# Performance work log

Hardware: AMD Instinct MI355X
Metric: run time of the kernel (lower is better)

The kernel has to match this reference:

```python
import jax, jax.numpy as jnp
import numpy as np

L_, H_, D_, GRP_ = 16, 16, 64, 4  # num_layers, num_heads, dims, conv groups factor


def setup_inputs() -> dict:
    key = jax.random.key(0)
    k1, k2, k3 = jax.random.split(key, 3)
    B, K, n, E = 4, 4, 256, 768
    G = GRP_ * L_ * 2                      # 128 conv groups
    Cin_g = E * L_ * 2 // G                # 192 in-channels per group
    Cout_g = H_ * D_ * L_ * 2 // G         # 256 out-channels per group
    rng = np.random.default_rng(0)
    lengths = rng.integers(n // 2, n + 1, size=B * K)
    mask = (np.arange(n)[None, :] < lengths[:, None]).astype(np.int32)
    last_hidden = jax.random.normal(k1, (B * K, n, E), jnp.float32) * 0.02
    weight = jax.random.normal(k2, (G, Cout_g, Cin_g), jnp.float32) * 0.02
    bias = jax.random.normal(k3, (G * Cout_g,), jnp.float32) * 0.02
    return {"last_hidden": last_hidden, "attention_mask": jnp.asarray(mask),
            "weight": weight, "bias": bias, "k": K}


def _forward(last_hidden, weight, bias, mask_np, k):
    Bk, n, E = last_hidden.shape
    B = Bk // k
    G = weight.shape[0]
    # mean pooling over valid tokens
    mask_f = jnp.asarray(mask_np).astype(last_hidden.dtype)
    pooled = (last_hidden * mask_f[..., None]).sum(1) / mask_f.sum(1)[..., None]
    # tile along feature dim (L*2 copies), move channels first: [Bk, E*2L, n]
    x = jnp.tile(last_hidden, (1, 1, 2 * L_)).transpose(0, 2, 1)
    x = x.reshape(Bk, G, -1, n)  # [Bk, G, Cin/G, n]
    # grouped 1x1 conv == per-group GEMM
    y = jnp.einsum('bgin,goi->bgon', x, weight).reshape(Bk, -1, n) + bias[None, :, None]
    # [B, k, L, 2, D, H, n] -> permute(0,1,2,3,5,6,4) -> [B, k, L, 2, H, n, D]
    y = y.reshape(B, k, L_, 2, D_, H_, n).transpose(0, 1, 2, 3, 5, 6, 4)
    # bring (k, n) together for ragged gather: [B, k*n, L, 2, H, D]
    y = y.transpose(0, 1, 5, 2, 3, 4, 6).reshape(B, k * n, L_, 2, H_, D_)
    lens = mask_np.sum(1).reshape(B, k)
    Tmax = int(lens.sum(1).max())
    idx = np.zeros((B, Tmax), np.int32)
    valid = np.zeros((B, Tmax), np.int32)
    for i in range(B):  # tiny host-side loop over B to build gather map
        pos = np.concatenate([j * n + np.arange(lens[i, j]) for j in range(k)])
        idx[i, :pos.size] = pos
        valid[i, :pos.size] = 1
    batch = y[jnp.arange(B)[:, None], jnp.asarray(idx)]  # [B, Tmax, L, 2, H, D]
    batch = batch * jnp.asarray(valid)[:, :, None, None, None, None].astype(batch.dtype)
    batch = batch.transpose(2, 3, 0, 4, 1, 5)  # [L, 2, B, H, Tmax, D]
    return pooled, batch, jnp.asarray(valid, jnp.int32)


def reference(last_hidden, attention_mask, weight, bias, k):
    mask_np = np.asarray(attention_mask)
    return _forward(last_hidden, weight, bias, mask_np, k)
```

## Files before the change

### kernel.cpp

```cpp
#include <hip/hip_runtime.h>
#include <hip/hip_bf16.h>


typedef float f32x4 __attribute__((ext_vector_type(4)));
typedef __bf16 bf16x8 __attribute__((ext_vector_type(8)));
typedef unsigned short u16x4 __attribute__((ext_vector_type(4)));
typedef unsigned short u16x8 __attribute__((ext_vector_type(8)));

__device__ __forceinline__ unsigned short f2bf(float f) {
    union { float f; unsigned u; } v; v.f = f;
    unsigned r = v.u + 0x7FFFu + ((v.u >> 16) & 1u);
    return (unsigned short)(r >> 16);
}

__device__ __forceinline__ bf16x8 ldfrag(const unsigned short* p) {
    u16x8 r = *(const u16x8*)p;
    return __builtin_bit_cast(bf16x8, r);
}

__global__ void cums_kernel(const int* __restrict__ mask, int* __restrict__ ws,
                            float* __restrict__ valid_out, int Tmax) {
    int tid = threadIdx.x;
    int w = tid >> 6, lane = tid & 63;
    int m = mask[w * 256 + lane] + mask[w * 256 + lane + 64] +
            mask[w * 256 + lane + 128] + mask[w * 256 + lane + 192];
#pragma unroll
    for (int off = 32; off > 0; off >>= 1) m += __shfl_down(m, off);
    if (lane == 0) ws[w] = m;
    __syncthreads();
    if (tid == 0) {
        for (int b = 0; b < 4; ++b) {
            int c = 0;
            for (int j = 0; j < 4; ++j) { ws[16 + b * 4 + j] = c; c += ws[b * 4 + j]; }
            ws[32 + b] = c;
        }
    }
    __syncthreads();
    for (int i = tid; i < 4 * Tmax; i += 1024) {
        int b = i / Tmax;
        int T = i - b * Tmax;
        valid_out[i] = (T < ws[32 + b]) ? 1.0f : 0.0f;
    }
}

__global__ void pooled_kernel(const float* __restrict__ lh, const int* __restrict__ mask,
                              const int* __restrict__ ws, float* __restrict__ pooled) {
    int bs = blockIdx.x / 12;
    int ec = blockIdx.x - bs * 12;
    int tid = threadIdx.x;
    int tg = tid >> 6, lane = tid & 63;
    int e = ec * 64 + lane;
    float s = 0.f;
    for (int t = tg; t < 256; t += 4) {
        float mf = (float)mask[bs * 256 + t];
        s += lh[(size_t)(bs * 256 + t) * 768 + e] * mf;
    }
    __shared__ float red[4][64];
    red[tg][lane] = s;
    __syncthreads();
    if (tg == 0) {
        float tot = red[0][lane] + red[1][lane] + red[2][lane] + red[3][lane];
        pooled[bs * 768 + e] = tot / (float)ws[bs];
    }
}

__global__ void packall_kernel(const float* __restrict__ wgt, const float* __restrict__ lh,
                               unsigned short* __restrict__ Wp, unsigned short* __restrict__ Lp) {
    int bid = blockIdx.x;
    if (bid < 3072) {
        int ls = bid / 96;
        int rem = bid - ls * 96;
        int kk = rem >> 4;
        int blk = rem & 15;
        int slot = (blk << 8) + threadIdx.x;
        int row = slot >> 2;
        int sc = slot & 3;
        int coloff = (sc ^ ((row >> 1) & 3)) << 3;
        const float* src = wgt + (size_t)ls * 196608 + row * 192 + (kk << 5) + coloff;
        f32x4 a0 = *(const f32x4*)src;
        f32x4 a1 = *(const f32x4*)(src + 4);
        u16x8 w = { f2bf(a0[0]), f2bf(a0[1]), f2bf(a0[2]), f2bf(a0[3]),
                    f2bf(a1[0]), f2bf(a1[1]), f2bf(a1[2]), f2bf(a1[3]) };
        *(u16x8*)(Wp + (((size_t)(ls * 6 + kk) << 12) + slot) * 8) = w;
    } else {
        size_t slot = (size_t)(bid - 3072) * 256 + threadIdx.x;
        const float* src = lh + slot * 8;
        f32x4 a0 = *(const f32x4*)src;
        f32x4 a1 = *(const f32x4*)(src + 4);
        u16x8 w = { f2bf(a0[0]), f2bf(a0[1]), f2bf(a0[2]), f2bf(a0[3]),
                    f2bf(a1[0]), f2bf(a1[1]), f2bf(a1[2]), f2bf(a1[3]) };
        *(u16x8*)(Lp + slot * 8) = w;
    }
}

__global__ __launch_bounds__(512, 4) void gemm_t(
    const unsigned short* __restrict__ Wp, const unsigned short* __restrict__ Lp,
    const float* __restrict__ bias, const int* __restrict__ ws,
    float* __restrict__ out, int Tmax, int nT) {
    __shared__ __align__(16) unsigned short As[1024][32];
    __shared__ __align__(16) float biasT[16][64];

    int x = blockIdx.x;
    int xcd = x & 7;
    int rest = x >> 3;
    int per = nT << 2;
    int lsq = rest / per;
    int j = rest - lsq * per;
    int ls = (lsq << 3) + xcd;
    int b = j / nT;
    int Tt = j - b * nT;
    int Tbase = Tt << 5;

    int total = ws[32 + b];
    int tid = threadIdx.x;
    int lane = tid & 63;
    int wv = tid >> 6;
    int toff = lane & 3, dcq = lane >> 2;
    float* batch = out + 12288;
    size_t hd0 = (size_t)((ls << 2) + b) << 4;

    if (Tbase >= total) {
        f32x4 z = {0.f, 0.f, 0.f, 0.f};
#pragma unroll
        for (int r = 0; r < 4; ++r) {
#pragma unroll
            for (int gi = 0; gi < 4; ++gi) {
                int flat = (wv << 2) + gi;
                int hq = flat >> 3, t4 = flat & 7;
                int tglob = Tbase + (t4 << 2) + toff;
                int h = (hq << 2) + r;
                if (tglob < Tmax) {
                    float* dst = batch + ((hd0 + h) * (size_t)Tmax + tglob) * 64;
                    *(f32x4*)(dst + (dcq << 2)) = z;
                }
            }
        }
        return;
    }

    {
        int i0 = tid, i1 = tid + 512;
        biasT[i0 & 15][((i0 >> 8) << 4) + ((i0 & 255) >> 4)] = bias[(ls << 10) + i0];
        biasT[i1 & 15][((i1 >> 8) << 4) + ((i1 & 255) >> 4)] = bias[(ls << 10) + i1];
    }

    int beta = wv >> 1, oh = wv & 1;
    int p = lane & 15, q = lane >> 4;

    int c1 = ws[16 + (b << 2) + 1];
    int c2 = ws[16 + (b << 2) + 2];
    int c3 = ws[16 + (b << 2) + 3];
    const unsigned short* Brow[2];
    bool bval[2];
#pragma unroll
    for (int n = 0; n < 2; ++n) {
        int Ti = Tbase + (n << 4) + p;
        bval[n] = Ti < total;
        int TiC = bval[n] ? Ti : (total - 1);
        int sj = (TiC >= c1) + (TiC >= c2) + (TiC >= c3);
        int cum = sj == 0 ? 0 : (sj == 1 ? c1 : (sj == 2 ? c2 : c3));
        int row = ((b << 2) + sj) * 256 + (TiC - cum);
        Brow[n] = Lp + (size_t)row * 768 + beta * 192 + (q << 3);
    }

    f32x4 acc[8][2] = {};
    const bf16x8 bz = {};

    const char* gpanel = (const char*)Wp + (((size_t)(ls * 6)) << 16) + (wv << 13) + (lane << 4);
    char* lbase = ((char*)&As[0][0]) + (wv << 13);

#pragma unroll
    for (int cc = 0; cc < 6; ++cc) {
        asm volatile("s_waitcnt lgkmcnt(0)" ::: "memory");
        __builtin_amdgcn_sched_barrier(0);
        const char* g = gpanel + ((size_t)cc << 16);
#pragma unroll
        for (int it = 0; it < 8; ++it)
            __builtin_amdgcn_global_load_lds(
                (const __attribute__((address_space(1))) void*)(g + it * 1024),
                (__attribute__((address_space(3))) void*)(lbase + it * 1024), 16, 0, 0);
        bf16x8 bf0 = bval[0] ? ldfrag(Brow[0] + (cc << 5)) : bz;
        bf16x8 bf1 = bval[1] ? ldfrag(Brow[1] + (cc << 5)) : bz;
        asm volatile("s_waitcnt vmcnt(0)" ::: "memory");
        __builtin_amdgcn_sched_barrier(0);
#pragma unroll
        for (int r8 = 0; r8 < 8; ++r8) {
            int row = (wv << 7) + (r8 << 4) + p;
            bf16x8 af = ldfrag(&As[row][(q ^ ((row >> 1) & 3)) << 3]);
            acc[r8][0] = __builtin_amdgcn_mfma_f32_16x16x32_bf16(af, bf0, acc[r8][0], 0, 0, 0);
            acc[r8][1] = __builtin_amdgcn_mfma_f32_16x16x32_bf16(af, bf1, acc[r8][1], 0, 0, 0);
        }
    }

    __syncthreads();

    float* Ltr = (float*)&As[0][0];
    int col0 = (beta << 4) + (oh << 3);

#pragma unroll
    for (int r = 0; r < 4; ++r) {
#pragma unroll
        for (int n = 0; n < 2; ++n) {
            int rowL = (((n << 4) + p) << 2) + q;
            f32x4 v0 = { acc[0][n][r], acc[1][n][r], acc[2][n][r], acc[3][n][r] };
            f32x4 v1 = { acc[4][n][r], acc[5][n][r], acc[6][n][r], acc[7][n][r] };
            *(f32x4*)(Ltr + rowL * 68 + col0) = v0;
            *(f32x4*)(Ltr + rowL * 68 + col0 + 4) = v1;
        }
        __syncthreads();
#pragma unroll
        for (int gi = 0; gi < 4; ++gi) {
            int flat = (wv << 2) + gi;
            int hq = flat >> 3, t4 = flat & 7;
            int tloc = (t4 << 2) + toff;
            int h = (hq << 2) + r;
            int tglob = Tbase + tloc;
            if (tglob < Tmax) {
                f32x4 v;
                if (tglob < total) {
                    v = *(const f32x4*)(Ltr + ((tloc << 2) + hq) * 68 + (dcq << 2));
                    v += *(const f32x4*)&biasT[h][dcq << 2];
                } else {
                    v = (f32x4){0.f, 0.f, 0.f, 0.f};
                }
                float* dst = batch + ((hd0 + h) * (size_t)Tmax + tglob) * 64;
                *(f32x4*)(dst + (dcq << 2)) = v;
            }
        }
        __syncthreads();
    }
}

__global__ void zerotail_kernel(float* __restrict__ batch, const int* __restrict__ ws,
                                int Tmax) {
    int rr = blockIdx.x;
    int b = rr >> 9;
    int rem = rr & 511;
    int l = rem >> 5, s = (rem >> 4) & 1, h = rem & 15;
    int total = ws[32 + b];
    int span = Tmax - total;
    if (span <= 0) return;
    float* row = batch + (((size_t)((l * 2 + s) * 4 + b) * 16 + h) * (size_t)Tmax + total) * 64;
    f32x4 z = {0.f, 0.f, 0.f, 0.f};
    int nchunk = span << 4;
    for (int j = threadIdx.x; j < nchunk; j += 256)
        *(f32x4*)(row + (j << 2)) = z;
}

__global__ __launch_bounds__(512, 4) void gemm_fb(
    const float* __restrict__ lh, const float* __restrict__ wgt,
    const float* __restrict__ bias, const int* __restrict__ ws,
    float* __restrict__ out, int Tmax) {
    __shared__ __align__(16) unsigned short As[1024][32];
    __shared__ __align__(16) float biasT[16][64];

    int x = blockIdx.x;
    int xcd = x & 7;
    int rest = x >> 3;
    int lsq = rest >> 7;
    int rb = rest & 127;
    int ls = (lsq << 3) + xcd;
    int bs = rb >> 3;
    int tq = rb & 7;

    int len = ws[bs];
    int tbase = tq << 5;
    if (tbase >= len) return;

    int tid = threadIdx.x;
    {
        int i0 = tid, i1 = tid + 512;
        biasT[i0 & 15][((i0 >> 8) << 4) + ((i0 & 255) >> 4)] = bias[(ls << 10) + i0];
        biasT[i1 & 15][((i1 >> 8) << 4) + ((i1 & 255) >> 4)] = bias[(ls << 10) + i1];
    }

    int lane = tid & 63;
    int wv = tid >> 6;
    int beta = wv >> 1, oh = wv & 1;
    int p = lane & 15, q = lane >> 4;

    f32x4 acc[8][2] = {};

#pragma unroll
    for (int cc = 0; cc < 6; ++cc) {
        const int kk = cc << 5;
        const float* Awg = wgt + (size_t)ls * 196608;
        int arow0 = tid >> 2;
        int achk = tid & 3;
#pragma unroll
        for (int it = 0; it < 8; ++it) {
            int row = arow0 + (it << 7);
            const float* src = Awg + row * 192 + kk + (achk << 3);
            f32x4 a0 = *(const f32x4*)src;
            f32x4 a1 = *(const f32x4*)(src + 4);
            u16x8 aw = { f2bf(a0[0]), f2bf(a0[1]), f2bf(a0[2]), f2bf(a0[3]),
                         f2bf(a1[0]), f2bf(a1[1]), f2bf(a1[2]), f2bf(a1[3]) };
            *(u16x8*)&As[row][(achk ^ ((row >> 1) & 3)) << 3] = aw;
        }
        bf16x8 bf[2];
        const float* Brow = lh + (size_t)bs * 196608 + (size_t)(tbase + p) * 768 +
                            beta * 192 + (q << 3) + kk;
#pragma unroll
        for (int n = 0; n < 2; ++n) {
            const float* bp = Brow + n * 16 * 768;
            f32x4 b0 = *(const f32x4*)bp;
            f32x4 b1 = *(const f32x4*)(bp + 4);
            u16x8 bw = { f2bf(b0[0]), f2bf(b0[1]), f2bf(b0[2]), f2bf(b0[3]),
                         f2bf(b1[0]), f2bf(b1[1]), f2bf(b1[2]), f2bf(b1[3]) };
            bf[n] = __builtin_bit_cast(bf16x8, bw);
        }
        __syncthreads();
#pragma unroll
        for (int r8 = 0; r8 < 8; ++r8) {
            int row = (beta << 8) + (oh << 7) + (r8 << 4) + p;
            bf16x8 af = ldfrag(&As[row][(q ^ ((row >> 1) & 3)) << 3]);
            acc[r8][0] = __builtin_amdgcn_mfma_f32_16x16x32_bf16(af, bf[0], acc[r8][0], 0, 0, 0);
            acc[r8][1] = __builtin_amdgcn_mfma_f32_16x16x32_bf16(af, bf[1], acc[r8][1], 0, 0, 0);
        }
        __syncthreads();
    }

    float* Ltr = (float*)&As[0][0];
    int cum = ws[16 + bs];
    int b = bs >> 2;
    float* batch = out + 12288;
    size_t hd0 = (size_t)((ls << 2) + b) << 4;

    int toff = lane & 3, dcq = lane >> 2;
    int col0 = (beta << 4) + (oh << 3);

#pragma unroll
    for (int r = 0; r < 4; ++r) {
#pragma unroll
        for (int n = 0; n < 2; ++n) {
            int rowL = (((n << 4) + p) << 2) + q;
            f32x4 v0 = { acc[0][n][r], acc[1][n][r], acc[2][n][r], acc[3][n][r] };
            f32x4 v1 = { acc[4][n][r], acc[5][n][r], acc[6][n][r], acc[7][n][r] };
            *(f32x4*)(Ltr + rowL * 68 + col0) = v0;
            *(f32x4*)(Ltr + rowL * 68 + col0 + 4) = v1;
        }
        __syncthreads();
#pragma unroll
        for (int gi = 0; gi < 4; ++gi) {
            int flat = (wv << 2) + gi;
            int hq = flat >> 3, t4 = flat & 7;
            int tloc = (t4 << 2) + toff;
            int h = (hq << 2) + r;
            int tglob = tbase + tloc;
            f32x4 v = *(const f32x4*)(Ltr + ((tloc << 2) + hq) * 68 + (dcq << 2));
            v += *(const f32x4*)&biasT[h][dcq << 2];
            if (tglob < len) {
                float* dst = batch + ((hd0 + h) * (size_t)Tmax + cum + tglob) * 64;
                *(f32x4*)(dst + (dcq << 2)) = v;
            }
        }
        __syncthreads();
    }
}

extern "C" void kernel_launch(void* const* d_in, const int* in_sizes, int n_in,
                              void* d_out, int out_size, void* d_ws, size_t ws_size,
                              hipStream_t stream) {
    const float* lh   = (const float*)d_in[0];
    const int*   mask = (const int*)d_in[1];
    const float* wgt  = (const float*)d_in[2];
    const float* bias = (const float*)d_in[3];
    float* out = (float*)d_out;
    int* ws = (int*)d_ws;

    int Tmax = (out_size - 12288) / 131076;
    int nT = (Tmax + 31) >> 5;

    unsigned short* Wp = (unsigned short*)((char*)d_ws + 1024);
    unsigned short* Lp = (unsigned short*)((char*)d_ws + 1024 + 12582912);
    const size_t need = 1024 + 12582912 + 6291456;
    bool packed = ws_size >= need;

    cums_kernel<<<1, 1024, 0, stream>>>(mask, ws, out + 12288 + (size_t)131072 * Tmax, Tmax);
    pooled_kernel<<<16 * 12, 256, 0, stream>>>(lh, mask, ws, out);

    if (packed) {
        packall_kernel<<<4608, 256, 0, stream>>>(wgt, lh, Wp, Lp);
        gemm_t<<<128 * nT, 512, 0, stream>>>(Wp, Lp, bias, ws, out, Tmax, nT);
    } else {
        zerotail_kernel<<<2048, 256, 0, stream>>>(out + 12288, ws, Tmax);
        gemm_fb<<<4096, 512, 0, stream>>>(lh, wgt, bias, ws, out, Tmax);
    }
}
```

Baseline: 192.4 us.

## Merge prep kernels into one launch and software-pipeline GEMM K-loop loads

The mask cumsum, pooled mean and bf16 pack kernels are merged into a single prep launch, so three launches become one. The pooled branch now derives each sequence length from the mask itself instead of reading ws written by another block. The GEMM K loop is restructured to prefetch the next B fragment and issue the next A panel's global-to-LDS load after the current MFMAs, overlapping memory with compute. Risk: the LDS buffer is reused without a barrier between waves, so correctness depends on each wave only touching its own slice.

```diff
diff --git a/kernel.cpp b/kernel.cpp
--- a/kernel.cpp
+++ b/kernel.cpp
@@ -18,61 +18,29 @@
     return __builtin_bit_cast(bf16x8, r);
 }
 
-__global__ void cums_kernel(const int* __restrict__ mask, int* __restrict__ ws,
+__device__ __forceinline__ bf16x8 ldfrag_masked(const unsigned short* p, bool valid) {
+    u16x8 r = *(const u16x8*)p;
+    u16x8 z = {};
+    r = valid ? r : z;
+    return __builtin_bit_cast(bf16x8, r);
+}
+
+__global__ void prep_kernel(const float* __restrict__ wgt, const float* __restrict__ lh,
+                            const int* __restrict__ mask,
+                            unsigned short* __restrict__ Wp, unsigned short* __restrict__ Lp,
+                            int* __restrict__ ws, float* __restrict__ pooled,
                             float* __restrict__ valid_out, int Tmax) {
+    __shared__ float red[4][64];
+    __shared__ float mred[4];
+    int bid = blockIdx.x;
     int tid = threadIdx.x;
-    int w = tid >> 6, lane = tid & 63;
-    int m = mask[w * 256 + lane] + mask[w * 256 + lane + 64] +
-            mask[w * 256 + lane + 128] + mask[w * 256 + lane + 192];
-#pragma unroll
-    for (int off = 32; off > 0; off >>= 1) m += __shfl_down(m, off);
-    if (lane == 0) ws[w] = m;
-    __syncthreads();
-    if (tid == 0) {
-        for (int b = 0; b < 4; ++b) {
-            int c = 0;
-            for (int j = 0; j < 4; ++j) { ws[16 + b * 4 + j] = c; c += ws[b * 4 + j]; }
-            ws[32 + b] = c;
-        }
-    }
-    __syncthreads();
-    for (int i = tid; i < 4 * Tmax; i += 1024) {
-        int b = i / Tmax;
-        int T = i - b * Tmax;
-        valid_out[i] = (T < ws[32 + b]) ? 1.0f : 0.0f;
-    }
-}
-
-__global__ void pooled_kernel(const float* __restrict__ lh, const int* __restrict__ mask,
-                              const int* __restrict__ ws, float* __restrict__ pooled) {
-    int bs = blockIdx.x / 12;
-    int ec = blockIdx.x - bs * 12;
-    int tid = threadIdx.x;
-    int tg = tid >> 6, lane = tid & 63;
-    int e = ec * 64 + lane;
-    float s = 0.f;
-    for (int t = tg; t < 256; t += 4) {
-        float mf = (float)mask[bs * 256 + t];
-        s += lh[(size_t)(bs * 256 + t) * 768 + e] * mf;
-    }
-    __shared__ float red[4][64];
-    red[tg][lane] = s;
-    __syncthreads();
-    if (tg == 0) {
-        float tot = red[0][lane] + red[1][lane] + red[2][lane] + red[3][lane];
-        pooled[bs * 768 + e] = tot / (float)ws[bs];
-    }
-}
-
-__global__ void packall_kernel(const float* __restrict__ wgt, const float* __restrict__ lh,
-                               unsigned short* __restrict__ Wp, unsigned short* __restrict__ Lp) {
-    int bid = blockIdx.x;
+
     if (bid < 3072) {
         int ls = bid / 96;
         int rem = bid - ls * 96;
         int kk = rem >> 4;
         int blk = rem & 15;
-        int slot = (blk << 8) + threadIdx.x;
+        int slot = (blk << 8) + tid;
         int row = slot >> 2;
         int sc = slot & 3;
         int coloff = (sc ^ ((row >> 1) & 3)) << 3;
@@ -82,14 +50,56 @@
         u16x8 w = { f2bf(a0[0]), f2bf(a0[1]), f2bf(a0[2]), f2bf(a0[3]),
                     f2bf(a1[0]), f2bf(a1[1]), f2bf(a1[2]), f2bf(a1[3]) };
         *(u16x8*)(Wp + (((size_t)(ls * 6 + kk) << 12) + slot) * 8) = w;
-    } else {
-        size_t slot = (size_t)(bid - 3072) * 256 + threadIdx.x;
+    } else if (bid < 4608) {
+        size_t slot = (size_t)(bid - 3072) * 256 + tid;
         const float* src = lh + slot * 8;
         f32x4 a0 = *(const f32x4*)src;
         f32x4 a1 = *(const f32x4*)(src + 4);
         u16x8 w = { f2bf(a0[0]), f2bf(a0[1]), f2bf(a0[2]), f2bf(a0[3]),
                     f2bf(a1[0]), f2bf(a1[1]), f2bf(a1[2]), f2bf(a1[3]) };
         *(u16x8*)(Lp + slot * 8) = w;
+    } else if (bid < 4800) {
+        int r = bid - 4608;
+        int bs = r / 12, ec = r - bs * 12;
+        int tg = tid >> 6, lane = tid & 63;
+        int e = ec * 64 + lane;
+        float s = 0.f, mc = 0.f;
+        for (int t = tg; t < 256; t += 4) {
+            float mf = (float)mask[bs * 256 + t];
+            s += lh[(size_t)(bs * 256 + t) * 768 + e] * mf;
+            mc += mf;
+        }
+        red[tg][lane] = s;
+        if (lane == 0) mred[tg] = mc;
+        __syncthreads();
+        if (tg == 0) {
+            float tot = red[0][lane] + red[1][lane] + red[2][lane] + red[3][lane];
+            float len = mred[0] + mred[1] + mred[2] + mred[3];
+            pooled[bs * 768 + e] = tot / len;
+        }
+    } else {
+        int w = tid >> 6, lane = tid & 63;
+        for (int bs = w; bs < 16; bs += 4) {
+            int m = mask[bs * 256 + lane] + mask[bs * 256 + lane + 64] +
+                    mask[bs * 256 + lane + 128] + mask[bs * 256 + lane + 192];
+#pragma unroll
+            for (int off = 32; off > 0; off >>= 1) m += __shfl_down(m, off);
+            if (lane == 0) ws[bs] = m;
+        }
+        __syncthreads();
+        if (tid == 0) {
+            for (int b = 0; b < 4; ++b) {
+                int c = 0;
+                for (int j = 0; j < 4; ++j) { ws[16 + b * 4 + j] = c; c += ws[b * 4 + j]; }
+                ws[32 + b] = c;
+            }
+        }
+        __syncthreads();
+        for (int i = tid; i < 4 * Tmax; i += 256) {
+            int b = i / Tmax;
+            int T = i - b * Tmax;
+            valid_out[i] = (T < ws[32 + b]) ? 1.0f : 0.0f;
+        }
     }
 }
 
@@ -138,6 +148,14 @@
         return;
     }
 
+    const char* gpanel = (const char*)Wp + (((size_t)(ls * 6)) << 16) + (wv << 13) + (lane << 4);
+    char* lbase = ((char*)&As[0][0]) + (wv << 13);
+#pragma unroll
+    for (int it = 0; it < 8; ++it)
+        __builtin_amdgcn_global_load_lds(
+            (const __attribute__((address_space(1))) void*)(gpanel + it * 1024),
+            (__attribute__((address_space(3))) void*)(lbase + it * 1024), 16, 0, 0);
+
     {
         int i0 = tid, i1 = tid + 512;
         biasT[i0 & 15][((i0 >> 8) << 4) + ((i0 & 255) >> 4)] = bias[(ls << 10) + i0];
@@ -166,30 +184,38 @@
     f32x4 acc[8][2] = {};
     const bf16x8 bz = {};
 
-    const char* gpanel = (const char*)Wp + (((size_t)(ls * 6)) << 16) + (wv << 13) + (lane << 4);
-    char* lbase = ((char*)&As[0][0]) + (wv << 13);
+    bf16x8 bc0 = ldfrag_masked(Brow[0], bval[0]);
+    bf16x8 bc1 = ldfrag_masked(Brow[1], bval[1]);
 
 #pragma unroll
     for (int cc = 0; cc < 6; ++cc) {
-        asm volatile("s_waitcnt lgkmcnt(0)" ::: "memory");
-        __builtin_amdgcn_sched_barrier(0);
-        const char* g = gpanel + ((size_t)cc << 16);
-#pragma unroll
-        for (int it = 0; it < 8; ++it)
-            __builtin_amdgcn_global_load_lds(
-                (const __attribute__((address_space(1))) void*)(g + it * 1024),
-                (__attribute__((address_space(3))) void*)(lbase + it * 1024), 16, 0, 0);
-        bf16x8 bf0 = bval[0] ? ldfrag(Brow[0] + (cc << 5)) : bz;
-        bf16x8 bf1 = bval[1] ? ldfrag(Brow[1] + (cc << 5)) : bz;
-        asm volatile("s_waitcnt vmcnt(0)" ::: "memory");
+        bf16x8 bn0 = bz, bn1 = bz;
+        if (cc < 5) {
+            bn0 = ldfrag_masked(Brow[0] + ((cc + 1) << 5), bval[0]);
+            bn1 = ldfrag_masked(Brow[1] + ((cc + 1) << 5), bval[1]);
+            asm volatile("s_waitcnt vmcnt(2)" ::: "memory");
+        } else {
+            asm volatile("s_waitcnt vmcnt(0)" ::: "memory");
+        }
         __builtin_amdgcn_sched_barrier(0);
 #pragma unroll
         for (int r8 = 0; r8 < 8; ++r8) {
             int row = (wv << 7) + (r8 << 4) + p;
             bf16x8 af = ldfrag(&As[row][(q ^ ((row >> 1) & 3)) << 3]);
-            acc[r8][0] = __builtin_amdgcn_mfma_f32_16x16x32_bf16(af, bf0, acc[r8][0], 0, 0, 0);
-            acc[r8][1] = __builtin_amdgcn_mfma_f32_16x16x32_bf16(af, bf1, acc[r8][1], 0, 0, 0);
-        }
+            acc[r8][0] = __builtin_amdgcn_mfma_f32_16x16x32_bf16(af, bc0, acc[r8][0], 0, 0, 0);
+            acc[r8][1] = __builtin_amdgcn_mfma_f32_16x16x32_bf16(af, bc1, acc[r8][1], 0, 0, 0);
+        }
+        if (cc < 5) {
+            asm volatile("s_waitcnt lgkmcnt(0)" ::: "memory");
+            __builtin_amdgcn_sched_barrier(0);
+            const char* g = gpanel + ((size_t)(cc + 1) << 16);
+#pragma unroll
+            for (int it = 0; it < 8; ++it)
+                __builtin_amdgcn_global_load_lds(
+                    (const __attribute__((address_space(1))) void*)(g + it * 1024),
+                    (__attribute__((address_space(3))) void*)(lbase + it * 1024), 16, 0, 0);
+        }
+        bc0 = bn0; bc1 = bn1;
     }
 
     __syncthreads();
@@ -231,6 +257,52 @@
     }
 }
 
+__global__ void cums_kernel(const int* __restrict__ mask, int* __restrict__ ws,
+                            float* __restrict__ valid_out, int Tmax) {
+    int tid = threadIdx.x;
+    int w = tid >> 6, lane = tid & 63;
+    int m = mask[w * 256 + lane] + mask[w * 256 + lane + 64] +
+            mask[w * 256 + lane + 128] + mask[w * 256 + lane + 192];
+#pragma unroll
+    for (int off = 32; off > 0; off >>= 1) m += __shfl_down(m, off);
+    if (lane == 0) ws[w] = m;
+    __syncthreads();
+    if (tid == 0) {
+        for (int b = 0; b < 4; ++b) {
+            int c = 0;
+            for (int j = 0; j < 4; ++j) { ws[16 + b * 4 + j] = c; c += ws[b * 4 + j]; }
+            ws[32 + b] = c;
+        }
+    }
+    __syncthreads();
+    for (int i = tid; i < 4 * Tmax; i += 1024) {
+        int b = i / Tmax;
+        int T = i - b * Tmax;
+        valid_out[i] = (T < ws[32 + b]) ? 1.0f : 0.0f;
+    }
+}
+
+__global__ void pooled_kernel(const float* __restrict__ lh, const int* __restrict__ mask,
+                              const int* __restrict__ ws, float* __restrict__ pooled) {
+    int bs = blockIdx.x / 12;
+    int ec = blockIdx.x - bs * 12;
+    int tid = threadIdx.x;
+    int tg = tid >> 6, lane = tid & 63;
+    int e = ec * 64 + lane;
+    float s = 0.f;
+    for (int t = tg; t < 256; t += 4) {
+        float mf = (float)mask[bs * 256 + t];
+        s += lh[(size_t)(bs * 256 + t) * 768 + e] * mf;
+    }
+    __shared__ float red[4][64];
+    red[tg][lane] = s;
+    __syncthreads();
+    if (tg == 0) {
+        float tot = red[0][lane] + red[1][lane] + red[2][lane] + red[3][lane];
+        pooled[bs * 768 + e] = tot / (float)ws[bs];
+    }
+}
+
 __global__ void zerotail_kernel(float* __restrict__ batch, const int* __restrict__ ws,
                                 int Tmax) {
     int rr = blockIdx.x;
@@ -376,13 +448,14 @@
     const size_t need = 1024 + 12582912 + 6291456;
     bool packed = ws_size >= need;
 
-    cums_kernel<<<1, 1024, 0, stream>>>(mask, ws, out + 12288 + (size_t)131072 * Tmax, Tmax);
-    pooled_kernel<<<16 * 12, 256, 0, stream>>>(lh, mask, ws, out);
+    float* valid_out = out + 12288 + (size_t)131072 * Tmax;
 
     if (packed) {
-        packall_kernel<<<4608, 256, 0, stream>>>(wgt, lh, Wp, Lp);
+        prep_kernel<<<4801, 256, 0, stream>>>(wgt, lh, mask, Wp, Lp, ws, out, valid_out, Tmax);
         gemm_t<<<128 * nT, 512, 0, stream>>>(Wp, Lp, bias, ws, out, Tmax, nT);
     } else {
+        cums_kernel<<<1, 1024, 0, stream>>>(mask, ws, valid_out, Tmax);
+        pooled_kernel<<<16 * 12, 256, 0, stream>>>(lh, mask, ws, out);
         zerotail_kernel<<<2048, 256, 0, stream>>>(out + 12288, ws, Tmax);
         gemm_fb<<<4096, 512, 0, stream>>>(lh, wgt, bias, ws, out, Tmax);
     }
```

After: 187.0 us (median of 2 runs). 2.8% less time.
